# Optimization experiments

Measured on AMD Instinct MI355X. Metric: run time of the kernel, lower is better.

## Reference

```python
import jax, jax.numpy as jnp
import numpy as np

B, H, W, C = 4, 64, 64, 512
EPS = 1e-3  # keras BatchNormalization default epsilon


def setup_inputs() -> dict:
    key = jax.random.key(0)
    ks = jax.random.split(key, 16)
    c8, c2 = C // 8, C // 2
    sc = lambda fan_in: 1.0 / np.sqrt(fan_in)
    inp = {
        "x": jax.random.normal(ks[0], (B, H, W, C), dtype=jnp.float32),
        # 1x1 conv weights as [Cin, Cout] matrices
        "wf": jax.random.normal(ks[1], (C, c8), dtype=jnp.float32) * sc(C),
        "bf": jnp.zeros((c8,), jnp.float32),
        "wg": jax.random.normal(ks[2], (C, c8), dtype=jnp.float32) * sc(C),
        "bg": jnp.zeros((c8,), jnp.float32),
        "wh": jax.random.normal(ks[3], (C, c2), dtype=jnp.float32) * sc(C),
        "bh": jnp.zeros((c2,), jnp.float32),
        "wo": jax.random.normal(ks[4], (c2, C), dtype=jnp.float32) * sc(c2),
        "bo": jnp.zeros((C,), jnp.float32),
        "gamma": jax.random.normal(ks[5], (1,), dtype=jnp.float32) * 0.05,
        # concat 1x1 conv (2C -> C), has bias (use_batchnorm=False default)
        "wc": jax.random.normal(ks[6], (2 * C, C), dtype=jnp.float32) * sc(2 * C),
        "bc": jnp.zeros((C,), jnp.float32),
        # BN inference params (moving statistics)
        "bn_scale": jnp.ones((C,), jnp.float32),
        "bn_bias": jnp.zeros((C,), jnp.float32),
        "bn_mean": jnp.zeros((C,), jnp.float32),
        "bn_var": jnp.ones((C,), jnp.float32),
    }
    return inp


def reference(x, wf, bf, wg, bg, wh, bh, wo, bo, gamma, wc, bc,
              bn_scale, bn_bias, bn_mean, bn_var):
    b, h, w, c = x.shape
    n = h * w
    xf = x.reshape(b, n, c)
    f = xf @ wf + bf          # [B, N, C/8]
    g = xf @ wg + bg          # [B, N, C/8]
    hv = xf @ wh + bh         # [B, N, C/2]
    s = jnp.einsum('bnd,bmd->bnm', g, f)   # [B, N, N]
    beta = jax.nn.softmax(s, axis=-1)
    o = jnp.einsum('bnm,bmd->bnd', beta, hv)  # [B, N, C/2]
    o = o @ wo + bo                            # [B, N, C]
    att = gamma * o + xf                       # gamma-scaled residual
    cat = jnp.concatenate([att, xf], axis=-1)  # [B, N, 2C]
    y = cat @ wc + bc
    # BatchNorm inference + relu
    y = (y - bn_mean) * (bn_scale / jnp.sqrt(bn_var + EPS)) + bn_bias
    y = jax.nn.relu(y)
    return y.reshape(b, h, w, c)
```

## Files before the change

kernel.cpp:

```cpp
#include <hip/hip_runtime.h>
#include <hip/hip_bf16.h>

typedef __bf16 bf16x8 __attribute__((ext_vector_type(8)));
typedef float f32x4 __attribute__((ext_vector_type(4)));

#define EPSBN 1e-3f

constexpr int NPIX = 4096;
constexpr int D2 = 256;

#define RAW_BARRIER() do { \
  asm volatile("s_waitcnt lgkmcnt(0)" ::: "memory"); \
  __builtin_amdgcn_s_barrier(); \
  asm volatile("" ::: "memory"); \
} while (0)

__global__ __launch_bounds__(256) void k_cvt(const float* __restrict__ x,
                                             __bf16* __restrict__ xb, int n4) {
  int i = blockIdx.x * 256 + threadIdx.x;
  if (i >= n4) return;
  float4 v = reinterpret_cast<const float4*>(x)[i];
  union { __bf16 h[4]; uint2 u; } o;
  o.h[0] = (__bf16)v.x; o.h[1] = (__bf16)v.y; o.h[2] = (__bf16)v.z; o.h[3] = (__bf16)v.w;
  reinterpret_cast<uint2*>(xb)[i] = o.u;
}

__global__ __launch_bounds__(256) void kp_wfgh(const float* __restrict__ wf,
                                               const float* __restrict__ wg,
                                               const float* __restrict__ wh,
                                               __bf16* __restrict__ WT) {
  int idx = blockIdx.x * 256 + threadIdx.x;
  int c = idx >> 9, k = idx & 511;
  float v = (c < 64) ? wf[k * 64 + c] : (c < 128) ? wg[k * 64 + (c - 64)] : wh[k * 256 + (c - 128)];
  WT[idx] = (__bf16)v;
}

__global__ __launch_bounds__(128) void kp_bias384(const float* bf_, const float* bg_,
                                                  const float* bh_, float* bias) {
  int c = blockIdx.x * 128 + threadIdx.x;
  bias[c] = (c < 64) ? bf_[c] : (c < 128) ? bg_[c - 64] : bh_[c - 128];
}

__global__ __launch_bounds__(256) void kp_wow(const float* __restrict__ wo,
                                              const float* __restrict__ wc,
                                              float* __restrict__ Wow) {
  int idx = blockIdx.x * 256 + threadIdx.x;
  int d = idx >> 9, c = idx & 511;
  float a0 = 0.f, a1 = 0.f, a2 = 0.f, a3 = 0.f;
  for (int j = 0; j < 512; j += 4) {
    float4 w4 = *reinterpret_cast<const float4*>(wo + d * 512 + j);
    a0 += w4.x * wc[(size_t)j * 512 + c];
    a1 += w4.y * wc[(size_t)(j + 1) * 512 + c];
    a2 += w4.z * wc[(size_t)(j + 2) * 512 + c];
    a3 += w4.w * wc[(size_t)(j + 3) * 512 + c];
  }
  Wow[idx] = (a0 + a1) + (a2 + a3);
}

__global__ __launch_bounds__(256) void kp_wcat(const float* __restrict__ Wow,
                                               const float* __restrict__ wc,
                                               const float* __restrict__ gamma,
                                               const float* __restrict__ bns,
                                               const float* __restrict__ bnv,
                                               __bf16* __restrict__ WT) {
  int idx = blockIdx.x * 256 + threadIdx.x;
  int c = idx / 768, k = idx % 768;
  float s = bns[c] * rsqrtf(bnv[c] + EPSBN);
  float v;
  if (k < 256) v = gamma[0] * Wow[k * 512 + c] * s;
  else { int kk = k - 256; v = (wc[kk * 512 + c] + wc[(512 + kk) * 512 + c]) * s; }
  WT[idx] = (__bf16)v;
}

__global__ __launch_bounds__(256) void kp_biasF(const float* bo, const float* wc, const float* bc,
                                                const float* gamma, const float* bns, const float* bnb,
                                                const float* bnm, const float* bnv, float* biasF) {
  int c = blockIdx.x * 256 + threadIdx.x;
  float s = bns[c] * rsqrtf(bnv[c] + EPSBN);
  float a0 = 0.f, a1 = 0.f, a2 = 0.f, a3 = 0.f;
  for (int j = 0; j < 512; j += 4) {
    a0 += bo[j] * wc[(size_t)j * 512 + c];
    a1 += bo[j + 1] * wc[(size_t)(j + 1) * 512 + c];
    a2 += bo[j + 2] * wc[(size_t)(j + 2) * 512 + c];
    a3 += bo[j + 3] * wc[(size_t)(j + 3) * 512 + c];
  }
  float pre = bc[c] + gamma[0] * ((a0 + a1) + (a2 + a3));
  biasF[c] = (pre - bnm[c]) * s + bnb[c];
}

template <int KT, int NC, int MODE>
__global__ __launch_bounds__(256) void k_gemm(const __bf16* __restrict__ A1, int k1, int lda1,
                                              const __bf16* __restrict__ A2, int lda2,
                                              const __bf16* __restrict__ WT,
                                              const float* __restrict__ bias,
                                              void* __restrict__ out1,
                                              void* __restrict__ out2) {
  __shared__ __bf16 As[128][72];
  __shared__ __bf16 Ws[64][72];
  const int m0 = blockIdx.x * 128, n0 = blockIdx.y * 64;
  const int tid = threadIdx.x, lane = tid & 63, w = tid >> 6;
  const int wr = w >> 1, wcl = w & 1;
  const int l15 = lane & 15, l4 = lane >> 4;
  f32x4 acc[4][2] = {};
  for (int ks = 0; ks < KT; ks += 64) {
    const __bf16* Asrc; int lda, kb;
    if (ks < k1) { Asrc = A1; lda = lda1; kb = ks; }
    else         { Asrc = A2; lda = lda2; kb = ks - k1; }
#pragma unroll
    for (int it = 0; it < 4; ++it) {
      int idx = it * 256 + tid, r = idx >> 3, ch = idx & 7;
      *(bf16x8*)(&As[r][ch * 8]) = *(const bf16x8*)(Asrc + (size_t)(m0 + r) * lda + kb + ch * 8);
    }
#pragma unroll
    for (int it = 0; it < 2; ++it) {
      int idx = it * 256 + tid, r = idx >> 3, ch = idx & 7;
      *(bf16x8*)(&Ws[r][ch * 8]) = *(const bf16x8*)(WT + (size_t)(n0 + r) * KT + ks + ch * 8);
    }
    __syncthreads();
#pragma unroll
    for (int kk = 0; kk < 2; ++kk) {
      int krd = kk * 32 + l4 * 8;
      bf16x8 av[4], bv[2];
#pragma unroll
      for (int mi = 0; mi < 4; ++mi) av[mi] = *(const bf16x8*)(&As[wr * 64 + mi * 16 + l15][krd]);
#pragma unroll
      for (int ni = 0; ni < 2; ++ni) bv[ni] = *(const bf16x8*)(&Ws[wcl * 32 + ni * 16 + l15][krd]);
#pragma unroll
      for (int mi = 0; mi < 4; ++mi)
#pragma unroll
        for (int ni = 0; ni < 2; ++ni)
          acc[mi][ni] = __builtin_amdgcn_mfma_f32_16x16x32_bf16(av[mi], bv[ni], acc[mi][ni], 0, 0, 0);
    }
    __syncthreads();
  }
#pragma unroll
  for (int mi = 0; mi < 4; ++mi)
#pragma unroll
    for (int ni = 0; ni < 2; ++ni) {
      int col = n0 + wcl * 32 + ni * 16 + l15;
      float bcol = bias[col];
      int row0 = m0 + wr * 64 + mi * 16 + l4 * 4;
      if (MODE == 1) {
        float* out = (float*)out1;
#pragma unroll
        for (int r = 0; r < 4; ++r)
          out[(size_t)(row0 + r) * NC + col] = fmaxf(acc[mi][ni][r] + bcol, 0.f);
      } else {
        if (col < 128) {
          __bf16* fg = (__bf16*)out1;
#pragma unroll
          for (int r = 0; r < 4; ++r)
            fg[(size_t)(row0 + r) * 128 + col] = (__bf16)(acc[mi][ni][r] + bcol);
        } else {
          __bf16* hvT = (__bf16*)out2;
          int bb = row0 >> 12, n = row0 & 4095;
          union { __bf16 h[4]; uint2 u; } pk;
#pragma unroll
          for (int r = 0; r < 4; ++r) pk.h[r] = (__bf16)(acc[mi][ni][r] + bcol);
          *(uint2*)(hvT + ((size_t)(bb * 256 + (col - 128))) * 4096 + n) = pk.u;
        }
      }
    }
}

__global__ __launch_bounds__(512, 4) void k_attn(const __bf16* __restrict__ fg,
                                                 const __bf16* __restrict__ hvT,
                                                 __bf16* __restrict__ obuf) {
  __shared__ __bf16 PsT[2][64][136];
  __shared__ float Lp[8][64];
  const int id = blockIdx.x;
  const int xcd = id & 7, i2 = id >> 3;
  const int b = xcd >> 1;
  const int dh = i2 & 1;
  const int q0 = ((i2 >> 1) * 2 + (xcd & 1)) * 64;
  const int tid = threadIdx.x, w = tid >> 6, lane = tid & 63;
  const int l15 = lane & 15, l4 = lane >> 4;
  const int dcol = dh * 128 + w * 16;
  const __bf16* fgb = fg + (size_t)b * NPIX * 128;
  const __bf16* vb = hvT + (size_t)b * D2 * NPIX;

  bf16x8 bG[4][2];
#pragma unroll
  for (int qt = 0; qt < 4; ++qt)
#pragma unroll
    for (int kk = 0; kk < 2; ++kk)
      bG[qt][kk] = *(const bf16x8*)(fgb + (size_t)(q0 + qt * 16 + l15) * 128 + 64 + kk * 32 + l4 * 8);

  bf16x8 aF[2], bV[4];
#pragma unroll
  for (int kk = 0; kk < 2; ++kk)
    aF[kk] = *(const bf16x8*)(fgb + (size_t)(w * 16 + l15) * 128 + kk * 32 + l4 * 8);
#pragma unroll
  for (int k4 = 0; k4 < 4; ++k4)
    bV[k4] = *(const bf16x8*)(vb + (size_t)(dcol + l15) * NPIX + k4 * 32 + l4 * 8);

  f32x4 accO[4] = {};
  float lsum[4] = {0.f, 0.f, 0.f, 0.f};

  for (int t = 0; t < 32; ++t) {
    const int mn = ((t + 1) * 128) & (NPIX - 1);
    const int bufi = t & 1;
    f32x4 s[4];
#pragma unroll
    for (int qt = 0; qt < 4; ++qt) {
      s[qt] = (f32x4){0.f, 0.f, 0.f, 0.f};
#pragma unroll
      for (int kk = 0; kk < 2; ++kk)
        s[qt] = __builtin_amdgcn_mfma_f32_16x16x32_bf16(aF[kk], bG[qt][kk], s[qt], 0, 0, 0);
    }
    bf16x8 aFn[2];
#pragma unroll
    for (int kk = 0; kk < 2; ++kk)
      aFn[kk] = *(const bf16x8*)(fgb + (size_t)(mn + w * 16 + l15) * 128 + kk * 32 + l4 * 8);
#pragma unroll
    for (int qt = 0; qt < 4; ++qt) {
      float p0 = __expf(s[qt][0]), p1 = __expf(s[qt][1]);
      float p2 = __expf(s[qt][2]), p3 = __expf(s[qt][3]);
      lsum[qt] += (p0 + p1) + (p2 + p3);
      union { __bf16 h[2]; uint u; } w0, w1;
      w0.h[0] = (__bf16)p0; w0.h[1] = (__bf16)p1;
      w1.h[0] = (__bf16)p2; w1.h[1] = (__bf16)p3;
      *(uint*)(&PsT[bufi][qt * 16 + l15][w * 16 + l4 * 4]) = w0.u;
      *(uint*)(&PsT[bufi][qt * 16 + l15][w * 16 + l4 * 4 + 2]) = w1.u;
    }
    RAW_BARRIER();
#pragma unroll
    for (int qt = 0; qt < 4; ++qt) {
      bf16x8 aP[4];
#pragma unroll
      for (int k4 = 0; k4 < 4; ++k4)
        aP[k4] = *(const bf16x8*)(&PsT[bufi][qt * 16 + l15][k4 * 32 + l4 * 8]);
#pragma unroll
      for (int k4 = 0; k4 < 4; ++k4)
        accO[qt] = __builtin_amdgcn_mfma_f32_16x16x32_bf16(aP[k4], bV[k4], accO[qt], 0, 0, 0);
    }
#pragma unroll
    for (int k4 = 0; k4 < 4; ++k4)
      bV[k4] = *(const bf16x8*)(vb + (size_t)(dcol + l15) * NPIX + mn + k4 * 32 + l4 * 8);
    aF[0] = aFn[0]; aF[1] = aFn[1];
  }

#pragma unroll
  for (int qt = 0; qt < 4; ++qt) {
    float v = lsum[qt];
    v += __shfl_xor(v, 16); v += __shfl_xor(v, 32);
    lsum[qt] = v;
  }
  if (l4 == 0) {
#pragma unroll
    for (int qt = 0; qt < 4; ++qt) Lp[w][qt * 16 + l15] = lsum[qt];
  }
  __syncthreads();
  float inv[4][4];
#pragma unroll
  for (int qt = 0; qt < 4; ++qt)
#pragma unroll
    for (int r = 0; r < 4; ++r) {
      int q = qt * 16 + l4 * 4 + r;
      float lt = 0.f;
#pragma unroll
      for (int ww = 0; ww < 8; ++ww) lt += Lp[ww][q];
      inv[qt][r] = 1.0f / lt;
    }
  __bf16* ob = obuf + ((size_t)b * NPIX + q0) * D2;
#pragma unroll
  for (int qt = 0; qt < 4; ++qt)
#pragma unroll
    for (int r = 0; r < 4; ++r)
      ob[(size_t)(qt * 16 + l4 * 4 + r) * D2 + dcol + l15] =
          (__bf16)(accO[qt][r] * inv[qt][r]);
}

extern "C" void kernel_launch(void* const* d_in, const int* in_sizes, int n_in,
                              void* d_out, int out_size, void* d_ws, size_t ws_size,
                              hipStream_t stream) {
  const float* x = (const float*)d_in[0];
  const float* wf = (const float*)d_in[1];
  const float* bf_ = (const float*)d_in[2];
  const float* wg = (const float*)d_in[3];
  const float* bg_ = (const float*)d_in[4];
  const float* wh = (const float*)d_in[5];
  const float* bh_ = (const float*)d_in[6];
  const float* wo = (const float*)d_in[7];
  const float* bo = (const float*)d_in[8];
  const float* gamma = (const float*)d_in[9];
  const float* wc = (const float*)d_in[10];
  const float* bc = (const float*)d_in[11];
  const float* bns = (const float*)d_in[12];
  const float* bnb = (const float*)d_in[13];
  const float* bnm = (const float*)d_in[14];
  const float* bnv = (const float*)d_in[15];
  (void)in_sizes; (void)n_in; (void)out_size; (void)ws_size;

  char* ws = (char*)d_ws;
  __bf16* xb     = (__bf16*)(ws + 0);
  __bf16* fg     = (__bf16*)(ws + 16777216);
  __bf16* hvT    = (__bf16*)(ws + 20971520);
  __bf16* obuf   = (__bf16*)(ws + 29360128);
  __bf16* WfghT  = (__bf16*)(ws + 37748736);
  float*  bias384= (float*) (ws + 38141952);
  float*  Wow    = (float*) (ws + 38143488);
  __bf16* WcatT  = (__bf16*)(ws + 38667776);
  float*  biasF  = (float*) (ws + 39454208);
  float* out = (float*)d_out;

  hipLaunchKernelGGL(k_cvt, dim3(8192), dim3(256), 0, stream, x, xb, 2097152);
  hipLaunchKernelGGL(kp_wfgh, dim3(768), dim3(256), 0, stream, wf, wg, wh, WfghT);
  hipLaunchKernelGGL(kp_bias384, dim3(3), dim3(128), 0, stream, bf_, bg_, bh_, bias384);
  hipLaunchKernelGGL(kp_wow, dim3(512), dim3(256), 0, stream, wo, wc, Wow);
  hipLaunchKernelGGL(kp_wcat, dim3(1536), dim3(256), 0, stream, Wow, wc, gamma, bns, bnv, WcatT);
  hipLaunchKernelGGL(kp_biasF, dim3(2), dim3(256), 0, stream, bo, wc, bc, gamma, bns, bnb, bnm, bnv, biasF);
  hipLaunchKernelGGL((k_gemm<512, 384, 0>), dim3(128, 6), dim3(256), 0, stream,
                     xb, 512, 512, xb, 512, WfghT, bias384, (void*)fg, (void*)hvT);
  hipLaunchKernelGGL(k_attn, dim3(512), dim3(512), 0, stream, fg, hvT, obuf);
  hipLaunchKernelGGL((k_gemm<768, 512, 1>), dim3(128, 8), dim3(256), 0, stream,
                     obuf, 256, 256, xb, 512, WcatT, biasF, (void*)out, nullptr);
}
```

Baseline: 283.6 us.

## Cover full value width per attention block and transpose hv stores via LDS

Each attention block now computes all 256 value columns for its 64 queries instead of splitting them into two halves across separate blocks. This halves the grid and stops the score/exp/softmax work from being done twice per query tile, at the cost of doubled accumulator and value-register pressure, so launch bounds drop to 2 blocks per SM. The value prefetch is double-buffered across two unrolled iterations. The projection GEMM also transposes its hv output tile through shared memory, so hvT is written with coalesced 16-byte stores instead of scattered 8-byte ones.

Result: faster. 269.7 us (-4.9%).

```diff
diff --git a/kernel.cpp b/kernel.cpp
--- a/kernel.cpp
+++ b/kernel.cpp
@@ -133,37 +133,61 @@
     }
     __syncthreads();
   }
-#pragma unroll
-  for (int mi = 0; mi < 4; ++mi)
-#pragma unroll
-    for (int ni = 0; ni < 2; ++ni) {
-      int col = n0 + wcl * 32 + ni * 16 + l15;
-      float bcol = bias[col];
-      int row0 = m0 + wr * 64 + mi * 16 + l4 * 4;
-      if (MODE == 1) {
+  if (MODE == 1) {
+#pragma unroll
+    for (int mi = 0; mi < 4; ++mi)
+#pragma unroll
+      for (int ni = 0; ni < 2; ++ni) {
+        int col = n0 + wcl * 32 + ni * 16 + l15;
+        float bcol = bias[col];
+        int row0 = m0 + wr * 64 + mi * 16 + l4 * 4;
         float* out = (float*)out1;
 #pragma unroll
         for (int r = 0; r < 4; ++r)
           out[(size_t)(row0 + r) * NC + col] = fmaxf(acc[mi][ni][r] + bcol, 0.f);
-      } else {
-        if (col < 128) {
-          __bf16* fg = (__bf16*)out1;
-#pragma unroll
-          for (int r = 0; r < 4; ++r)
-            fg[(size_t)(row0 + r) * 128 + col] = (__bf16)(acc[mi][ni][r] + bcol);
-        } else {
-          __bf16* hvT = (__bf16*)out2;
-          int bb = row0 >> 12, n = row0 & 4095;
-          union { __bf16 h[4]; uint2 u; } pk;
-#pragma unroll
-          for (int r = 0; r < 4; ++r) pk.h[r] = (__bf16)(acc[mi][ni][r] + bcol);
-          *(uint2*)(hvT + ((size_t)(bb * 256 + (col - 128))) * 4096 + n) = pk.u;
-        }
       }
-    }
-}
-
-__global__ __launch_bounds__(512, 4) void k_attn(const __bf16* __restrict__ fg,
+  } else if (n0 < 128) {
+#pragma unroll
+    for (int mi = 0; mi < 4; ++mi)
+#pragma unroll
+      for (int ni = 0; ni < 2; ++ni) {
+        int col = n0 + wcl * 32 + ni * 16 + l15;
+        float bcol = bias[col];
+        int row0 = m0 + wr * 64 + mi * 16 + l4 * 4;
+        __bf16* fg = (__bf16*)out1;
+#pragma unroll
+        for (int r = 0; r < 4; ++r)
+          fg[(size_t)(row0 + r) * 128 + col] = (__bf16)(acc[mi][ni][r] + bcol);
+      }
+  } else {
+    __syncthreads();
+    __bf16 (*Tt)[136] = (__bf16(*)[136])(&As[0][0]);
+#pragma unroll
+    for (int mi = 0; mi < 4; ++mi)
+#pragma unroll
+      for (int ni = 0; ni < 2; ++ni) {
+        int dloc = wcl * 32 + ni * 16 + l15;
+        float bcol = bias[n0 + dloc];
+        int nloc = wr * 64 + mi * 16 + l4 * 4;
+#pragma unroll
+        for (int r = 0; r < 4; ++r)
+          Tt[dloc][nloc + r] = (__bf16)(acc[mi][ni][r] + bcol);
+      }
+    __syncthreads();
+    const int bb = m0 >> 12, n = m0 & 4095, d0 = n0 - 128;
+    __bf16* hvT = (__bf16*)out2;
+    const int rrow = tid >> 3, c8 = tid & 7;
+#pragma unroll
+    for (int rep = 0; rep < 2; ++rep) {
+      int dl = rrow + rep * 32;
+      __bf16* dst = hvT + ((size_t)(bb * 256 + d0 + dl)) * 4096 + n;
+      *(bf16x8*)(dst + c8 * 8) = *(const bf16x8*)(&Tt[dl][c8 * 8]);
+      *(bf16x8*)(dst + 64 + c8 * 8) = *(const bf16x8*)(&Tt[dl][64 + c8 * 8]);
+    }
+  }
+}
+
+__global__ __launch_bounds__(512, 2) void k_attn(const __bf16* __restrict__ fg,
                                                  const __bf16* __restrict__ hvT,
                                                  __bf16* __restrict__ obuf) {
   __shared__ __bf16 PsT[2][64][136];
@@ -171,11 +195,9 @@
   const int id = blockIdx.x;
   const int xcd = id & 7, i2 = id >> 3;
   const int b = xcd >> 1;
-  const int dh = i2 & 1;
-  const int q0 = ((i2 >> 1) * 2 + (xcd & 1)) * 64;
+  const int q0 = (i2 * 2 + (xcd & 1)) * 64;
   const int tid = threadIdx.x, w = tid >> 6, lane = tid & 63;
   const int l15 = lane & 15, l4 = lane >> 4;
-  const int dcol = dh * 128 + w * 16;
   const __bf16* fgb = fg + (size_t)b * NPIX * 128;
   const __bf16* vb = hvT + (size_t)b * D2 * NPIX;
 
@@ -186,59 +208,73 @@
     for (int kk = 0; kk < 2; ++kk)
       bG[qt][kk] = *(const bf16x8*)(fgb + (size_t)(q0 + qt * 16 + l15) * 128 + 64 + kk * 32 + l4 * 8);
 
-  bf16x8 aF[2], bV[4];
+  bf16x8 aF[2], bVA[2][4], bVB[2][4];
 #pragma unroll
   for (int kk = 0; kk < 2; ++kk)
     aF[kk] = *(const bf16x8*)(fgb + (size_t)(w * 16 + l15) * 128 + kk * 32 + l4 * 8);
 #pragma unroll
-  for (int k4 = 0; k4 < 4; ++k4)
-    bV[k4] = *(const bf16x8*)(vb + (size_t)(dcol + l15) * NPIX + k4 * 32 + l4 * 8);
-
-  f32x4 accO[4] = {};
+  for (int dj = 0; dj < 2; ++dj)
+#pragma unroll
+    for (int k4 = 0; k4 < 4; ++k4) {
+      bVA[dj][k4] = *(const bf16x8*)(vb + (size_t)(w * 32 + dj * 16 + l15) * NPIX + k4 * 32 + l4 * 8);
+      bVB[dj][k4] = *(const bf16x8*)(vb + (size_t)(w * 32 + dj * 16 + l15) * NPIX + 128 + k4 * 32 + l4 * 8);
+    }
+
+  f32x4 accO[4][2] = {};
   float lsum[4] = {0.f, 0.f, 0.f, 0.f};
 
-  for (int t = 0; t < 32; ++t) {
-    const int mn = ((t + 1) * 128) & (NPIX - 1);
-    const int bufi = t & 1;
-    f32x4 s[4];
-#pragma unroll
-    for (int qt = 0; qt < 4; ++qt) {
-      s[qt] = (f32x4){0.f, 0.f, 0.f, 0.f};
-#pragma unroll
-      for (int kk = 0; kk < 2; ++kk)
-        s[qt] = __builtin_amdgcn_mfma_f32_16x16x32_bf16(aF[kk], bG[qt][kk], s[qt], 0, 0, 0);
-    }
-    bf16x8 aFn[2];
-#pragma unroll
-    for (int kk = 0; kk < 2; ++kk)
-      aFn[kk] = *(const bf16x8*)(fgb + (size_t)(mn + w * 16 + l15) * 128 + kk * 32 + l4 * 8);
-#pragma unroll
-    for (int qt = 0; qt < 4; ++qt) {
-      float p0 = __expf(s[qt][0]), p1 = __expf(s[qt][1]);
-      float p2 = __expf(s[qt][2]), p3 = __expf(s[qt][3]);
-      lsum[qt] += (p0 + p1) + (p2 + p3);
-      union { __bf16 h[2]; uint u; } w0, w1;
-      w0.h[0] = (__bf16)p0; w0.h[1] = (__bf16)p1;
-      w1.h[0] = (__bf16)p2; w1.h[1] = (__bf16)p3;
-      *(uint*)(&PsT[bufi][qt * 16 + l15][w * 16 + l4 * 4]) = w0.u;
-      *(uint*)(&PsT[bufi][qt * 16 + l15][w * 16 + l4 * 4 + 2]) = w1.u;
-    }
-    RAW_BARRIER();
-#pragma unroll
-    for (int qt = 0; qt < 4; ++qt) {
-      bf16x8 aP[4];
-#pragma unroll
-      for (int k4 = 0; k4 < 4; ++k4)
-        aP[k4] = *(const bf16x8*)(&PsT[bufi][qt * 16 + l15][k4 * 32 + l4 * 8]);
-#pragma unroll
-      for (int k4 = 0; k4 < 4; ++k4)
-        accO[qt] = __builtin_amdgcn_mfma_f32_16x16x32_bf16(aP[k4], bV[k4], accO[qt], 0, 0, 0);
-    }
-#pragma unroll
-    for (int k4 = 0; k4 < 4; ++k4)
-      bV[k4] = *(const bf16x8*)(vb + (size_t)(dcol + l15) * NPIX + mn + k4 * 32 + l4 * 8);
-    aF[0] = aFn[0]; aF[1] = aFn[1];
-  }
+#define ABODY(T, BV) do {                                                               \
+    const int mn1 = (((T) + 1) * 128) & (NPIX - 1);                                     \
+    const int mn2 = (((T) + 2) * 128) & (NPIX - 1);                                     \
+    const int bufi = (T) & 1;                                                           \
+    f32x4 s[4];                                                                         \
+    _Pragma("unroll")                                                                   \
+    for (int qt = 0; qt < 4; ++qt) {                                                    \
+      s[qt] = (f32x4){0.f, 0.f, 0.f, 0.f};                                              \
+      _Pragma("unroll")                                                                 \
+      for (int kk = 0; kk < 2; ++kk)                                                    \
+        s[qt] = __builtin_amdgcn_mfma_f32_16x16x32_bf16(aF[kk], bG[qt][kk], s[qt], 0, 0, 0); \
+    }                                                                                   \
+    bf16x8 aFn[2];                                                                      \
+    _Pragma("unroll")                                                                   \
+    for (int kk = 0; kk < 2; ++kk)                                                      \
+      aFn[kk] = *(const bf16x8*)(fgb + (size_t)(mn1 + w * 16 + l15) * 128 + kk * 32 + l4 * 8); \
+    _Pragma("unroll")                                                                   \
+    for (int qt = 0; qt < 4; ++qt) {                                                    \
+      float p0 = __expf(s[qt][0]), p1 = __expf(s[qt][1]);                               \
+      float p2 = __expf(s[qt][2]), p3 = __expf(s[qt][3]);                               \
+      lsum[qt] += (p0 + p1) + (p2 + p3);                                                \
+      union { __bf16 h[4]; uint2 u; } pk;                                               \
+      pk.h[0] = (__bf16)p0; pk.h[1] = (__bf16)p1;                                       \
+      pk.h[2] = (__bf16)p2; pk.h[3] = (__bf16)p3;                                       \
+      *(uint2*)(&PsT[bufi][qt * 16 + l15][w * 16 + l4 * 4]) = pk.u;                     \
+    }                                                                                   \
+    RAW_BARRIER();                                                                      \
+    _Pragma("unroll")                                                                   \
+    for (int qt = 0; qt < 4; ++qt) {                                                    \
+      bf16x8 aP[4];                                                                     \
+      _Pragma("unroll")                                                                 \
+      for (int k4 = 0; k4 < 4; ++k4)                                                    \
+        aP[k4] = *(const bf16x8*)(&PsT[bufi][qt * 16 + l15][k4 * 32 + l4 * 8]);         \
+      _Pragma("unroll")                                                                 \
+      for (int dj = 0; dj < 2; ++dj)                                                    \
+        _Pragma("unroll")                                                               \
+        for (int k4 = 0; k4 < 4; ++k4)                                                  \
+          accO[qt][dj] = __builtin_amdgcn_mfma_f32_16x16x32_bf16(aP[k4], BV[dj][k4], accO[qt][dj], 0, 0, 0); \
+    }                                                                                   \
+    _Pragma("unroll")                                                                   \
+    for (int dj = 0; dj < 2; ++dj)                                                      \
+      _Pragma("unroll")                                                                 \
+      for (int k4 = 0; k4 < 4; ++k4)                                                    \
+        BV[dj][k4] = *(const bf16x8*)(vb + (size_t)(w * 32 + dj * 16 + l15) * NPIX + mn2 + k4 * 32 + l4 * 8); \
+    aF[0] = aFn[0]; aF[1] = aFn[1];                                                     \
+  } while (0)
+
+  for (int t = 0; t < 32; t += 2) {
+    ABODY(t, bVA);
+    ABODY(t + 1, bVB);
+  }
+#undef ABODY
 
 #pragma unroll
   for (int qt = 0; qt < 4; ++qt) {
@@ -266,9 +302,11 @@
 #pragma unroll
   for (int qt = 0; qt < 4; ++qt)
 #pragma unroll
-    for (int r = 0; r < 4; ++r)
-      ob[(size_t)(qt * 16 + l4 * 4 + r) * D2 + dcol + l15] =
-          (__bf16)(accO[qt][r] * inv[qt][r]);
+    for (int dj = 0; dj < 2; ++dj)
+#pragma unroll
+      for (int r = 0; r < 4; ++r)
+        ob[(size_t)(qt * 16 + l4 * 4 + r) * D2 + w * 32 + dj * 16 + l15] =
+            (__bf16)(accO[qt][dj][r] * inv[qt][r]);
 }
 
 extern "C" void kernel_launch(void* const* d_in, const int* in_sizes, int n_in,
@@ -312,7 +350,7 @@
   hipLaunchKernelGGL(kp_biasF, dim3(2), dim3(256), 0, stream, bo, wc, bc, gamma, bns, bnb, bnm, bnv, biasF);
   hipLaunchKernelGGL((k_gemm<512, 384, 0>), dim3(128, 6), dim3(256), 0, stream,
                      xb, 512, 512, xb, 512, WfghT, bias384, (void*)fg, (void*)hvT);
-  hipLaunchKernelGGL(k_attn, dim3(512), dim3(512), 0, stream, fg, hvT, obuf);
+  hipLaunchKernelGGL(k_attn, dim3(256), dim3(512), 0, stream, fg, hvT, obuf);
   hipLaunchKernelGGL((k_gemm<768, 512, 1>), dim3(128, 8), dim3(256), 0, stream,
                      obuf, 256, 256, xb, 512, WcatT, biasF, (void*)out, nullptr);
 }
```
